# Kernel tuning notes

Measured on AMD Instinct MI355X. Metric: run time of the kernel, lower is better.

## Reference

```python
import jax, jax.numpy as jnp
import numpy as np

N_NODES = 50000
HEADS = 8
NEG_SLOPE = 0.2


def _gat_conv(x, W, a_src, a_dst, b, src, dst, n_nodes):
    """PyG GATConv forward, concat=False (mean over heads), self-loops already in (src, dst)."""
    H, C = a_src.shape
    xl = (x @ W).reshape(n_nodes, H, C)                      # [N, H, C]
    alpha_src = jnp.einsum('nhc,hc->nh', xl, a_src)          # [N, H]
    alpha_dst = jnp.einsum('nhc,hc->nh', xl, a_dst)          # [N, H]
    alpha = jax.nn.leaky_relu(alpha_src[src] + alpha_dst[dst], NEG_SLOPE)  # [E, H]
    # segment softmax over edges grouped by destination node
    amax = jax.ops.segment_max(alpha, dst, num_segments=n_nodes)           # [N, H]
    amax = jnp.where(jnp.isfinite(amax), amax, jnp.zeros_like(amax))
    ex = jnp.exp(alpha - jax.lax.stop_gradient(amax)[dst])                  # [E, H]
    denom = jax.ops.segment_sum(ex, dst, num_segments=n_nodes)             # [N, H]
    coef = ex / (denom[dst] + 1e-16)                                        # [E, H]
    msg = xl[src] * coef[:, :, None]                                        # [E, H, C]
    out = jax.ops.segment_sum(msg, dst, num_segments=n_nodes)              # [N, H, C]
    return out.mean(axis=1) + b                                             # [N, C]


def setup_inputs() -> dict:
    key = jax.random.key(0)
    ks = jax.random.split(key, 12)
    in_feats, h_feats, out_feats = 256, 64, 64
    n_edges = 800000
    x = jax.random.normal(ks[0], (N_NODES, in_feats), dtype=jnp.float32)
    edge_index = jax.random.randint(ks[1], (2, n_edges), 0, N_NODES, dtype=jnp.int64)
    # Glorot-ish init for weights
    def glorot(k, shape, fan):
        return jax.random.normal(k, shape, dtype=jnp.float32) * (1.0 / np.sqrt(fan))
    W1 = glorot(ks[2], (in_feats, HEADS * h_feats), in_feats)
    a_src1 = glorot(ks[3], (HEADS, h_feats), h_feats)
    a_dst1 = glorot(ks[4], (HEADS, h_feats), h_feats)
    b1 = jnp.zeros((h_feats,), dtype=jnp.float32)
    W2 = glorot(ks[5], (h_feats, HEADS * out_feats), h_feats)
    a_src2 = glorot(ks[6], (HEADS, out_feats), out_feats)
    a_dst2 = glorot(ks[7], (HEADS, out_feats), out_feats)
    b2 = jnp.zeros((out_feats,), dtype=jnp.float32)
    return {"x": x, "edge_index": edge_index,
            "W1": W1, "a_src1": a_src1, "a_dst1": a_dst1, "b1": b1,
            "W2": W2, "a_src2": a_src2, "a_dst2": a_dst2, "b2": b2}


def reference(x, edge_index, W1, a_src1, a_dst1, b1, W2, a_src2, a_dst2, b2):
    n = x.shape[0]
    # PyG GATConv add_self_loops=True (default): append self loops
    loops = jnp.arange(n, dtype=edge_index.dtype)
    src = jnp.concatenate([edge_index[0], loops])
    dst = jnp.concatenate([edge_index[1], loops])
    # F.dropout(p=0.6) is identity in eval mode
    h = _gat_conv(x, W1, a_src1, a_dst1, b1, src, dst, n)
    h = jax.nn.relu(h)
    out = _gat_conv(h, W2, a_src2, a_dst2, b2, src, dst, n)
    return out
```

## Files before the change

kernel.cpp:

```cpp
#include <hip/hip_runtime.h>

#define NN 50000
#define MPAD 50048
#define HD 8
#define CD 64
#define NHF 512
#define SCAN_B 256
#define NBLK ((NN + SCAN_B - 1) / SCAN_B)

typedef __attribute__((ext_vector_type(8))) short short8v;
typedef __attribute__((ext_vector_type(8))) unsigned short us8;
typedef __attribute__((ext_vector_type(4))) unsigned short us4;
typedef __attribute__((ext_vector_type(4))) float f32x4;
typedef __attribute__((ext_vector_type(8))) _Float16 h8;

__device__ inline unsigned short f32_to_bf16(float f) {
    unsigned int u = __float_as_uint(f);
    unsigned int r = (u + 0x7fffu + ((u >> 16) & 1u)) >> 16;
    return (unsigned short)r;
}
__device__ inline float bf16_to_f32(unsigned short h) {
    return __uint_as_float(((unsigned int)h) << 16);
}

__global__ void k_hist(const int* __restrict__ dst, int E, int* __restrict__ cnt) {
    int e = blockIdx.x * 256 + threadIdx.x;
    if (e < E) atomicAdd(&cnt[dst[e]], 1);
}

__global__ __launch_bounds__(SCAN_B) void k_block_sums(const int* __restrict__ cnt,
                                                       int* __restrict__ bsums) {
    __shared__ int sdata[4];
    int i = blockIdx.x * SCAN_B + threadIdx.x;
    int v = (i < NN) ? cnt[i] + 1 : 0;
#pragma unroll
    for (int off = 1; off < 64; off <<= 1) v += __shfl_xor(v, off);
    if ((threadIdx.x & 63) == 0) sdata[threadIdx.x >> 6] = v;
    __syncthreads();
    if (threadIdx.x == 0) bsums[blockIdx.x] = sdata[0] + sdata[1] + sdata[2] + sdata[3];
}

__global__ __launch_bounds__(SCAN_B) void k_scan_bsums(const int* __restrict__ bsums,
                                                       int* __restrict__ boffs, int nblk) {
    __shared__ int tmp[SCAN_B];
    int tid = threadIdx.x;
    int v = (tid < nblk) ? bsums[tid] : 0;
    tmp[tid] = v;
    __syncthreads();
    for (int off = 1; off < SCAN_B; off <<= 1) {
        int t = (tid >= off) ? tmp[tid - off] : 0;
        __syncthreads();
        tmp[tid] += t;
        __syncthreads();
    }
    if (tid < nblk) boffs[tid] = tmp[tid] - v;
}

__global__ __launch_bounds__(SCAN_B) void k_emit(const int* __restrict__ cnt,
                                                 const int* __restrict__ boffs,
                                                 int* __restrict__ row_ptr,
                                                 int* __restrict__ cursor,
                                                 int* __restrict__ csr_src) {
    __shared__ int tmp[SCAN_B];
    int tid = threadIdx.x;
    int i = blockIdx.x * SCAN_B + tid;
    int v = (i < NN) ? cnt[i] + 1 : 0;
    tmp[tid] = v;
    __syncthreads();
    for (int off = 1; off < SCAN_B; off <<= 1) {
        int t = (tid >= off) ? tmp[tid - off] : 0;
        __syncthreads();
        tmp[tid] += t;
        __syncthreads();
    }
    int base = boffs[blockIdx.x] + tmp[tid] - v;
    if (i < NN) {
        row_ptr[i] = base;
        csr_src[base] = i;
        cursor[i] = base + 1;
        if (i == NN - 1) row_ptr[NN] = base + v;
    }
}

__global__ void k_scatter(const int* __restrict__ src, const int* __restrict__ dst,
                          int E, int* __restrict__ cursor, int* __restrict__ csr_src) {
    int e = blockIdx.x * 256 + threadIdx.x;
    if (e < E) {
        int pos = atomicAdd(&cursor[dst[e]], 1);
        csr_src[pos] = src[e];
    }
}

__global__ void k_split_w(const float* __restrict__ W1, unsigned short* __restrict__ bht1,
                          unsigned short* __restrict__ blt1,
                          const float* __restrict__ W2, unsigned short* __restrict__ bht2,
                          unsigned short* __restrict__ blt2) {
    int idx = blockIdx.x * 256 + threadIdx.x;
    const int n1 = 256 * NHF;
    if (idx < n1) {
        int k = idx >> 9, n = idx & 511;
        float v = W1[idx];
        unsigned short hb = f32_to_bf16(v);
        blt1[n * 256 + k] = f32_to_bf16(v - bf16_to_f32(hb));
        bht1[n * 256 + k] = hb;
    } else if (idx < n1 + 64 * NHF) {
        int i2 = idx - n1;
        int k = i2 >> 9, n = i2 & 511;
        float v = W2[i2];
        unsigned short hb = f32_to_bf16(v);
        blt2[n * 64 + k] = f32_to_bf16(v - bf16_to_f32(hb));
        bht2[n * 64 + k] = hb;
    }
}

#define BM 128
#define BN 256
#define BKF 32
#define LDK 40

template<int SPLIT>
__global__ __launch_bounds__(512, 4) void k_gemm(
    const float* __restrict__ Af,
    const unsigned short* __restrict__ Aht,
    const unsigned short* __restrict__ Alt,
    const unsigned short* __restrict__ Bht,
    const unsigned short* __restrict__ Blt,
    const float* __restrict__ a_src, const float* __restrict__ a_dst,
    _Float16* __restrict__ C, float* __restrict__ asrc_out, float* __restrict__ adst_out,
    int M, int K)
{
    __shared__ unsigned short Ash[BM][LDK];
    __shared__ unsigned short Asl[BM][LDK];
    __shared__ unsigned short Bsh[BN][LDK];
    __shared__ unsigned short Bsl[BN][LDK];

    const int t = threadIdx.x;
    const int lane = t & 63;
    const int wid = t >> 6;
    const int wr = wid >> 2;
    const int wc = wid & 3;
    const int bm = blockIdx.x * BM;
    const int bn = blockIdx.y * BN;
    const int l15 = lane & 15;
    const int lg = lane >> 4;

    f32x4 acc[4][4];
#pragma unroll
    for (int mi = 0; mi < 4; ++mi)
#pragma unroll
        for (int ni = 0; ni < 4; ++ni)
            acc[mi][ni] = (f32x4){0.f, 0.f, 0.f, 0.f};

    const int srowA = t >> 2;
    const int skcA  = (t & 3) * 8;
    const int srowB = t >> 1;
    const int skcB  = (t & 1) * 16;

    for (int k0 = 0; k0 < K; k0 += BKF) {
        __syncthreads();
        if (SPLIT) {
            const int gr = bm + srowA;
            if (gr < M) {
                const float* ga = Af + (size_t)gr * K + k0 + skcA;
                float4 v0 = *(const float4*)ga;
                float4 v1 = *(const float4*)(ga + 4);
                us4 h0, l0, h1, l1;
                h0.x = f32_to_bf16(v0.x); l0.x = f32_to_bf16(v0.x - bf16_to_f32(h0.x));
                h0.y = f32_to_bf16(v0.y); l0.y = f32_to_bf16(v0.y - bf16_to_f32(h0.y));
                h0.z = f32_to_bf16(v0.z); l0.z = f32_to_bf16(v0.z - bf16_to_f32(h0.z));
                h0.w = f32_to_bf16(v0.w); l0.w = f32_to_bf16(v0.w - bf16_to_f32(h0.w));
                h1.x = f32_to_bf16(v1.x); l1.x = f32_to_bf16(v1.x - bf16_to_f32(h1.x));
                h1.y = f32_to_bf16(v1.y); l1.y = f32_to_bf16(v1.y - bf16_to_f32(h1.y));
                h1.z = f32_to_bf16(v1.z); l1.z = f32_to_bf16(v1.z - bf16_to_f32(h1.z));
                h1.w = f32_to_bf16(v1.w); l1.w = f32_to_bf16(v1.w - bf16_to_f32(h1.w));
                *(us4*)&Ash[srowA][skcA]     = h0;
                *(us4*)&Ash[srowA][skcA + 4] = h1;
                *(us4*)&Asl[srowA][skcA]     = l0;
                *(us4*)&Asl[srowA][skcA + 4] = l1;
            } else {
                us4 z = (us4){0, 0, 0, 0};
                *(us4*)&Ash[srowA][skcA]     = z;
                *(us4*)&Ash[srowA][skcA + 4] = z;
                *(us4*)&Asl[srowA][skcA]     = z;
                *(us4*)&Asl[srowA][skcA + 4] = z;
            }
        } else {
            const unsigned short* gah = Aht + (size_t)(bm + srowA) * K + k0 + skcA;
            const unsigned short* gal = Alt + (size_t)(bm + srowA) * K + k0 + skcA;
            *(us8*)&Ash[srowA][skcA] = *(const us8*)gah;
            *(us8*)&Asl[srowA][skcA] = *(const us8*)gal;
        }
        {
            const unsigned short* gbh = Bht + (size_t)(bn + srowB) * K + k0 + skcB;
            const unsigned short* gbl = Blt + (size_t)(bn + srowB) * K + k0 + skcB;
            *(us8*)&Bsh[srowB][skcB]     = *(const us8*)gbh;
            *(us8*)&Bsh[srowB][skcB + 8] = *(const us8*)(gbh + 8);
            *(us8*)&Bsl[srowB][skcB]     = *(const us8*)gbl;
            *(us8*)&Bsl[srowB][skcB + 8] = *(const us8*)(gbl + 8);
        }
        __syncthreads();

        short8v ah[4], al[4];
#pragma unroll
        for (int i = 0; i < 4; ++i) {
            ah[i] = *(const short8v*)&Ash[wr * 64 + i * 16 + l15][lg * 8];
            al[i] = *(const short8v*)&Asl[wr * 64 + i * 16 + l15][lg * 8];
        }
#pragma unroll
        for (int ni = 0; ni < 4; ++ni) {
            short8v bh = *(const short8v*)&Bsh[wc * 64 + ni * 16 + l15][lg * 8];
            short8v bl = *(const short8v*)&Bsl[wc * 64 + ni * 16 + l15][lg * 8];
#pragma unroll
            for (int mi = 0; mi < 4; ++mi) {
                acc[mi][ni] = __builtin_amdgcn_mfma_f32_16x16x32_bf16(ah[mi], bh, acc[mi][ni], 0, 0, 0);
                acc[mi][ni] = __builtin_amdgcn_mfma_f32_16x16x32_bf16(ah[mi], bl, acc[mi][ni], 0, 0, 0);
                acc[mi][ni] = __builtin_amdgcn_mfma_f32_16x16x32_bf16(al[mi], bh, acc[mi][ni], 0, 0, 0);
            }
        }
    }

    const int head_w = (bn >> 6) + wc;
    float ca[4], cd[4];
#pragma unroll
    for (int ni = 0; ni < 4; ++ni) {
        ca[ni] = a_src[head_w * 64 + ni * 16 + l15];
        cd[ni] = a_dst[head_w * 64 + ni * 16 + l15];
    }
#pragma unroll
    for (int mi = 0; mi < 4; ++mi) {
#pragma unroll
        for (int r = 0; r < 4; ++r) {
            int row = bm + wr * 64 + mi * 16 + lg * 4 + r;
            float ps = 0.f, pd = 0.f;
#pragma unroll
            for (int ni = 0; ni < 4; ++ni) {
                float cv = acc[mi][ni][r];
                int col = bn + wc * 64 + ni * 16 + l15;
                if (row < M) C[(size_t)row * NHF + col] = (_Float16)cv;
                ps += cv * ca[ni];
                pd += cv * cd[ni];
            }
#pragma unroll
            for (int off = 1; off < 16; off <<= 1) {
                ps += __shfl_xor(ps, off);
                pd += __shfl_xor(pd, off);
            }
            if (l15 == 0 && row < M) {
                asrc_out[row * HD + head_w] = ps;
                adst_out[row * HD + head_w] = pd;
            }
        }
    }
}

__global__ __launch_bounds__(256) void k_aggregate(
    const _Float16* __restrict__ xl, const float* __restrict__ asrc,
    const float* __restrict__ adst, const int* __restrict__ row_ptr,
    const int* __restrict__ csr_src, const float* __restrict__ bias,
    float* __restrict__ out, unsigned short* __restrict__ o_hi,
    unsigned short* __restrict__ o_lo, int mode)
{
    __shared__ float sh[4][NHF];
    const int wid  = threadIdx.x >> 6;
    const int lane = threadIdx.x & 63;
    const int n    = blockIdx.x * 4 + wid;
    const int head = lane >> 3;
    const int off  = lane * 8;

    const float ad = adst[n * HD + head];
    const int e0 = row_ptr[n];
    const int e1 = row_ptr[n + 1];

    float acc[8] = {};
    float s = 0.f;

    int e = e0;
    for (; e + 4 <= e1; e += 4) {
        int i0 = csr_src[e];
        int i1 = csr_src[e + 1];
        int i2 = csr_src[e + 2];
        int i3 = csr_src[e + 3];
        float a0 = asrc[i0 * HD + head];
        float a1 = asrc[i1 * HD + head];
        float a2 = asrc[i2 * HD + head];
        float a3 = asrc[i3 * HD + head];
        h8 v0 = *(const h8*)(xl + (size_t)i0 * NHF + off);
        h8 v1 = *(const h8*)(xl + (size_t)i1 * NHF + off);
        h8 v2 = *(const h8*)(xl + (size_t)i2 * NHF + off);
        h8 v3 = *(const h8*)(xl + (size_t)i3 * NHF + off);
        a0 += ad; a1 += ad; a2 += ad; a3 += ad;
        float p0 = __expf(a0 > 0.f ? a0 : 0.2f * a0);
        float p1 = __expf(a1 > 0.f ? a1 : 0.2f * a1);
        float p2 = __expf(a2 > 0.f ? a2 : 0.2f * a2);
        float p3 = __expf(a3 > 0.f ? a3 : 0.2f * a3);
        s += p0 + p1 + p2 + p3;
#pragma unroll
        for (int j = 0; j < 8; ++j) {
            acc[j] += p0 * (float)v0[j];
            acc[j] += p1 * (float)v1[j];
            acc[j] += p2 * (float)v2[j];
            acc[j] += p3 * (float)v3[j];
        }
    }
    for (; e < e1; ++e) {
        int i0 = csr_src[e];
        float a = asrc[i0 * HD + head] + ad;
        h8 vv = *(const h8*)(xl + (size_t)i0 * NHF + off);
        float p = __expf(a > 0.f ? a : 0.2f * a);
        s += p;
#pragma unroll
        for (int j = 0; j < 8; ++j) acc[j] += p * (float)vv[j];
    }

    const float inv = 1.f / (s + 1e-16f);
#pragma unroll
    for (int j = 0; j < 8; ++j) sh[wid][off + j] = acc[j] * inv;
    __syncthreads();

    float sum = 0.f;
#pragma unroll
    for (int h2 = 0; h2 < HD; ++h2) sum += sh[wid][h2 * CD + lane];
    float res = sum * 0.125f + bias[lane];
    if (mode) {
        res = fmaxf(res, 0.f);
        unsigned short hb = f32_to_bf16(res);
        o_hi[(size_t)n * CD + lane] = hb;
        o_lo[(size_t)n * CD + lane] = f32_to_bf16(res - bf16_to_f32(hb));
    } else {
        out[(size_t)n * CD + lane] = res;
    }
}

extern "C" void kernel_launch(void* const* d_in, const int* in_sizes, int n_in,
                              void* d_out, int out_size, void* d_ws, size_t ws_size,
                              hipStream_t stream) {
    const float* x   = (const float*)d_in[0];
    const int*   ei  = (const int*)d_in[1];
    const float* W1  = (const float*)d_in[2];
    const float* as1 = (const float*)d_in[3];
    const float* ad1 = (const float*)d_in[4];
    const float* b1  = (const float*)d_in[5];
    const float* W2  = (const float*)d_in[6];
    const float* as2 = (const float*)d_in[7];
    const float* ad2 = (const float*)d_in[8];
    const float* b2  = (const float*)d_in[9];

    const int E = in_sizes[1] / 2;
    const int* esrc = ei;
    const int* edst = ei + E;

    char* ws = (char*)d_ws;
    _Float16* xlh        = (_Float16*)ws;
    float* asrc          = (float*)(ws + 51200000);
    float* adst          = (float*)(ws + 52800000);
    unsigned short* Hh   = (unsigned short*)(ws + 54400000);
    unsigned short* Hl   = (unsigned short*)(ws + 60806144);
    int*   row_ptr       = (int*)(ws + 67212288);
    int*   cursor        = (int*)(ws + 67412480);
    int*   csr_src       = (int*)(ws + 67612480);
    unsigned short* Bht1 = (unsigned short*)(ws + 71012480);
    unsigned short* Blt1 = (unsigned short*)(ws + 71274624);
    unsigned short* Bht2 = (unsigned short*)(ws + 71536768);
    unsigned short* Blt2 = (unsigned short*)(ws + 71602304);
    int*   bsums         = (int*)(ws + 71667840);
    int*   boffs         = (int*)(ws + 71668736);

    hipMemsetAsync(cursor, 0, NN * sizeof(int), stream);
    k_hist<<<(E + 255) / 256, 256, 0, stream>>>(edst, E, cursor);
    k_block_sums<<<NBLK, SCAN_B, 0, stream>>>(cursor, bsums);
    k_scan_bsums<<<1, SCAN_B, 0, stream>>>(bsums, boffs, NBLK);
    k_emit<<<NBLK, SCAN_B, 0, stream>>>(cursor, boffs, row_ptr, cursor, csr_src);
    k_scatter<<<(E + 255) / 256, 256, 0, stream>>>(esrc, edst, E, cursor, csr_src);

    k_split_w<<<((256 + 64) * NHF + 255) / 256, 256, 0, stream>>>(W1, Bht1, Blt1,
                                                                  W2, Bht2, Blt2);

    dim3 gemm_grid(MPAD / BM, NHF / BN);

    k_gemm<1><<<gemm_grid, 512, 0, stream>>>(x, nullptr, nullptr, Bht1, Blt1, as1, ad1,
                                             xlh, asrc, adst, NN, 256);
    k_aggregate<<<NN / 4, 256, 0, stream>>>(xlh, asrc, adst, row_ptr, csr_src, b1,
                                            nullptr, Hh, Hl, 1);

    k_gemm<0><<<gemm_grid, 512, 0, stream>>>(nullptr, Hh, Hl, Bht2, Blt2, as2, ad2,
                                             xlh, asrc, adst, NN, 64);
    k_aggregate<<<NN / 4, 256, 0, stream>>>(xlh, asrc, adst, row_ptr, csr_src, b2,
                                            (float*)d_out, nullptr, nullptr, 0);
}
```

Baseline: 453.4 us.

## Load GEMM tiles directly into LDS in fragment order via global_load_lds

Changes the shared-memory layout of the GEMM tiles to a fragment-major format where each 16x32 MFMA fragment is stored contiguously in lane order. The bf16 A and B tiles are then loaded with global_load_lds (direct global-to-LDS DMA) instead of passing through registers. This is meant to cut register staging and VGPR pressure and to make the LDS reads conflict-free and contiguous. It drops the padded LDK layout and depends on the builtin's per-lane address mapping matching the fragment order.

Result: no change. 461.5 us (+1.8%).

```diff
diff --git a/kernel.cpp b/kernel.cpp
--- a/kernel.cpp
+++ b/kernel.cpp
@@ -22,6 +22,10 @@
 __device__ inline float bf16_to_f32(unsigned short h) {
     return __uint_as_float(((unsigned int)h) << 16);
 }
+
+#define GLDS16(g, l) __builtin_amdgcn_global_load_lds(                          \
+    (const __attribute__((address_space(1))) unsigned int*)(g),                 \
+    (__attribute__((address_space(3))) unsigned int*)(l), 16, 0, 0)
 
 __global__ void k_hist(const int* __restrict__ dst, int E, int* __restrict__ cnt) {
     int e = blockIdx.x * 256 + threadIdx.x;
@@ -116,7 +120,6 @@
 #define BM 128
 #define BN 256
 #define BKF 32
-#define LDK 40
 
 template<int SPLIT>
 __global__ __launch_bounds__(512, 4) void k_gemm(
@@ -129,10 +132,10 @@
     _Float16* __restrict__ C, float* __restrict__ asrc_out, float* __restrict__ adst_out,
     int M, int K)
 {
-    __shared__ unsigned short Ash[BM][LDK];
-    __shared__ unsigned short Asl[BM][LDK];
-    __shared__ unsigned short Bsh[BN][LDK];
-    __shared__ unsigned short Bsl[BN][LDK];
+    __shared__ unsigned short AshF[8 * 512];
+    __shared__ unsigned short AslF[8 * 512];
+    __shared__ unsigned short BshF[16 * 512];
+    __shared__ unsigned short BslF[16 * 512];
 
     const int t = threadIdx.x;
     const int lane = t & 63;
@@ -151,17 +154,21 @@
         for (int ni = 0; ni < 4; ++ni)
             acc[mi][ni] = (f32x4){0.f, 0.f, 0.f, 0.f};
 
-    const int srowA = t >> 2;
-    const int skcA  = (t & 3) * 8;
-    const int srowB = t >> 1;
-    const int skcB  = (t & 1) * 16;
+    const int gRow = lane & 15;
+    const int gChk = lane >> 4;
+    const int aReg   = t >> 6;
+    const int aSlot  = t & 63;
+    const int aRow   = aReg * 16 + (t & 15);
+    const int aChunk = (t >> 4) & 3;
 
     for (int k0 = 0; k0 < K; k0 += BKF) {
         __syncthreads();
         if (SPLIT) {
-            const int gr = bm + srowA;
+            const int gr = bm + aRow;
+            unsigned short* dh = &AshF[aReg * 512 + aSlot * 8];
+            unsigned short* dl = &AslF[aReg * 512 + aSlot * 8];
             if (gr < M) {
-                const float* ga = Af + (size_t)gr * K + k0 + skcA;
+                const float* ga = Af + (size_t)gr * K + k0 + aChunk * 8;
                 float4 v0 = *(const float4*)ga;
                 float4 v1 = *(const float4*)(ga + 4);
                 us4 h0, l0, h1, l1;
@@ -173,43 +180,37 @@
                 h1.y = f32_to_bf16(v1.y); l1.y = f32_to_bf16(v1.y - bf16_to_f32(h1.y));
                 h1.z = f32_to_bf16(v1.z); l1.z = f32_to_bf16(v1.z - bf16_to_f32(h1.z));
                 h1.w = f32_to_bf16(v1.w); l1.w = f32_to_bf16(v1.w - bf16_to_f32(h1.w));
-                *(us4*)&Ash[srowA][skcA]     = h0;
-                *(us4*)&Ash[srowA][skcA + 4] = h1;
-                *(us4*)&Asl[srowA][skcA]     = l0;
-                *(us4*)&Asl[srowA][skcA + 4] = l1;
+                *(us4*)dh = h0; *(us4*)(dh + 4) = h1;
+                *(us4*)dl = l0; *(us4*)(dl + 4) = l1;
             } else {
                 us4 z = (us4){0, 0, 0, 0};
-                *(us4*)&Ash[srowA][skcA]     = z;
-                *(us4*)&Ash[srowA][skcA + 4] = z;
-                *(us4*)&Asl[srowA][skcA]     = z;
-                *(us4*)&Asl[srowA][skcA + 4] = z;
+                *(us4*)dh = z; *(us4*)(dh + 4) = z;
+                *(us4*)dl = z; *(us4*)(dl + 4) = z;
             }
         } else {
-            const unsigned short* gah = Aht + (size_t)(bm + srowA) * K + k0 + skcA;
-            const unsigned short* gal = Alt + (size_t)(bm + srowA) * K + k0 + skcA;
-            *(us8*)&Ash[srowA][skcA] = *(const us8*)gah;
-            *(us8*)&Asl[srowA][skcA] = *(const us8*)gal;
-        }
-        {
-            const unsigned short* gbh = Bht + (size_t)(bn + srowB) * K + k0 + skcB;
-            const unsigned short* gbl = Blt + (size_t)(bn + srowB) * K + k0 + skcB;
-            *(us8*)&Bsh[srowB][skcB]     = *(const us8*)gbh;
-            *(us8*)&Bsh[srowB][skcB + 8] = *(const us8*)(gbh + 8);
-            *(us8*)&Bsl[srowB][skcB]     = *(const us8*)gbl;
-            *(us8*)&Bsl[srowB][skcB + 8] = *(const us8*)(gbl + 8);
+            const size_t ar = (size_t)(bm + wid * 16 + gRow) * K + k0 + gChk * 8;
+            GLDS16(Aht + ar, &AshF[wid * 512]);
+            GLDS16(Alt + ar, &AslF[wid * 512]);
+        }
+#pragma unroll
+        for (int j = 0; j < 2; ++j) {
+            const int q = wid * 2 + j;
+            const size_t br = (size_t)(bn + q * 16 + gRow) * K + k0 + gChk * 8;
+            GLDS16(Bht + br, &BshF[q * 512]);
+            GLDS16(Blt + br, &BslF[q * 512]);
         }
         __syncthreads();
 
         short8v ah[4], al[4];
 #pragma unroll
         for (int i = 0; i < 4; ++i) {
-            ah[i] = *(const short8v*)&Ash[wr * 64 + i * 16 + l15][lg * 8];
-            al[i] = *(const short8v*)&Asl[wr * 64 + i * 16 + l15][lg * 8];
+            ah[i] = *(const short8v*)&AshF[(wr * 4 + i) * 512 + lane * 8];
+            al[i] = *(const short8v*)&AslF[(wr * 4 + i) * 512 + lane * 8];
         }
 #pragma unroll
         for (int ni = 0; ni < 4; ++ni) {
-            short8v bh = *(const short8v*)&Bsh[wc * 64 + ni * 16 + l15][lg * 8];
-            short8v bl = *(const short8v*)&Bsl[wc * 64 + ni * 16 + l15][lg * 8];
+            short8v bh = *(const short8v*)&BshF[(wc * 4 + ni) * 512 + lane * 8];
+            short8v bl = *(const short8v*)&BslF[(wc * 4 + ni) * 512 + lane * 8];
 #pragma unroll
             for (int mi = 0; mi < 4; ++mi) {
                 acc[mi][ni] = __builtin_amdgcn_mfma_f32_16x16x32_bf16(ah[mi], bh, acc[mi][ni], 0, 0, 0);
```
